# Kernel optimization log

Hardware: AMD Instinct MI355X
Metric: run time of the kernel (lower is better)

The kernel has to match this reference:

```python
import jax, jax.numpy as jnp
import numpy as np

NUM_HEADS = 16
INPUT_DIM = 1024
ATTENTION_DIM = 1024
DEPTH = ATTENTION_DIM // NUM_HEADS
NEG = -(2.0 ** 32) + 1.0  # large negative used by the original masking


def setup_inputs() -> dict:
    key = jax.random.key(0)
    kq, kk, k1, k2, k3 = jax.random.split(key, 5)
    B, L = 4, 1024
    s = 1.0 / np.sqrt(INPUT_DIM)
    return {
        "query": jax.random.normal(kq, (B, L, INPUT_DIM), dtype=jnp.float32),
        "key": jax.random.normal(kk, (B, L, INPUT_DIM), dtype=jnp.float32),
        "Wq": jax.random.normal(k1, (INPUT_DIM, ATTENTION_DIM), dtype=jnp.float32) * s,
        "Wk": jax.random.normal(k2, (INPUT_DIM, ATTENTION_DIM), dtype=jnp.float32) * s,
        "Wv": jax.random.normal(k3, (INPUT_DIM, ATTENTION_DIM), dtype=jnp.float32) * s,
    }


def reference(query, key, Wq, Wk, Wv):
    B, Lq, _ = query.shape
    Lk = key.shape[1]
    q = query @ Wq  # [B, Lq, A]
    k = key @ Wk    # [B, Lk, A]
    v = key @ Wv
    # Faithful to torch: raw row-major reshape [B, L, A] -> [B*H, L, depth]
    q_ = q.reshape(-1, Lq, DEPTH)
    k_ = k.reshape(-1, Lk, DEPTH)
    v_ = v.reshape(-1, Lk, DEPTH)
    scores = jnp.einsum('bid,bjd->bij', q_, k_) / (DEPTH ** 0.5)  # [BH, Lq, Lk]
    # key padding mask, tiled head-major like torch.tile(key_mask, [H, 1])
    key_mask = jnp.sign(jnp.abs(key.sum(-1)))           # [B, Lk]
    key_mask = jnp.tile(key_mask, (NUM_HEADS, 1))        # [HB, Lk]
    scores = jnp.where(key_mask[:, None, :] == 0, NEG, scores)
    # causal mask
    tril = jnp.tril(jnp.ones((Lq, Lk), dtype=scores.dtype))
    scores = jnp.where(tril[None] == 0, NEG, scores)
    attn = jax.nn.softmax(scores, axis=-1)
    # query mask: original tiles to [HB, Lk, Lq] and multiplies elementwise,
    # i.e. masks the LAST axis with the query mask (requires Lq == Lk)
    query_mask = jnp.sign(jnp.abs(query.sum(-1)))        # [B, Lq]
    query_mask = jnp.tile(query_mask, (NUM_HEADS, 1))    # [HB, Lq]
    attn = attn * query_mask[:, None, :]
    # dropout is identity in eval mode
    out = attn @ v_                                      # [BH, Lq, depth]
    out = jnp.concatenate(jnp.split(out, NUM_HEADS, axis=0), axis=-1)  # [B, Lq, A]
    out = out + query
    norm = jnp.sqrt(jnp.sum(out * out, axis=-1, keepdims=True))
    out = out / jnp.maximum(norm, 1e-12)
    return out
```

## Files before the change

kernel.cpp:

```cpp
#include <hip/hip_runtime.h>
#include <cstdint>
#include <cstddef>


#define US unsigned short

typedef __attribute__((ext_vector_type(4))) float f32x4;
typedef __attribute__((ext_vector_type(8))) short bf16x8;
typedef __attribute__((ext_vector_type(8))) US ushort8_t;
typedef __attribute__((ext_vector_type(4))) US ushort4_t;

__device__ __forceinline__ US f2bf(float f) {
  union { float f; uint32_t u; } c; c.f = f;
  uint32_t u = c.u;
  return (US)((u + 0x7FFFu + ((u >> 16) & 1u)) >> 16);
}

__device__ __forceinline__ uint32_t cvtpk(float lo, float hi) {
  uint32_t r;
  asm("v_cvt_pk_bf16_f32 %0, %1, %2" : "=v"(r) : "v"(lo), "v"(hi));
  return r;
}

__device__ __forceinline__ void gld16(const void* g, void* l) {
  __builtin_amdgcn_global_load_lds(
      (const __attribute__((address_space(1))) uint32_t*)g,
      (__attribute__((address_space(3))) uint32_t*)l, 16, 0, 0);
}

__global__ __launch_bounds__(256) void prep(const float* __restrict__ q,
                                            const float* __restrict__ k,
                                            US* __restrict__ qb,
                                            US* __restrict__ kb,
                                            const float* __restrict__ Wq,
                                            const float* __restrict__ Wk,
                                            const float* __restrict__ Wv,
                                            US* __restrict__ Tq,
                                            US* __restrict__ Tk,
                                            US* __restrict__ Tv) {
  const int bid = blockIdx.x;
  if (bid < 8192) {
    uint32_t i = bid * 256u + threadIdx.x;
    const bool isq = i < 1048576u;
    const float4* src = (const float4*)(isq ? q : k);
    US* dst = isq ? qb : kb;
    uint32_t j = isq ? i : i - 1048576u;
    float4 v = src[j];
    ushort4_t o = { f2bf(v.x), f2bf(v.y), f2bf(v.z), f2bf(v.w) };
    *(ushort4_t*)(dst + (size_t)j * 4) = o;
    return;
  }
  const int rem = bid - 8192;
  const int z = rem >> 8;
  const int r8 = rem & 255;
  const float* W = (z == 0) ? Wq : (z == 1) ? Wk : Wv;
  US* T = (z == 0) ? Tq : (z == 1) ? Tk : Tv;
  __shared__ float tile[64][65];
  const int r0 = (r8 >> 4) * 64, c0 = (r8 & 15) * 64;
  const int tx = threadIdx.x & 63, ty = threadIdx.x >> 6;
  #pragma unroll
  for (int rr = ty; rr < 64; rr += 4)
    tile[rr][tx] = W[(size_t)(r0 + rr) * 1024 + c0 + tx];
  __syncthreads();
  #pragma unroll
  for (int rr = ty; rr < 64; rr += 4)
    T[(size_t)(c0 + rr) * 1024 + r0 + tx] = f2bf(tile[tx][rr]);
}

__global__ __launch_bounds__(256) void gemm_qkv(
    const US* __restrict__ qin, const US* __restrict__ kin,
    const US* __restrict__ WqT, const US* __restrict__ WkT,
    const US* __restrict__ WvT,
    US* __restrict__ qo, US* __restrict__ ko, US* __restrict__ vo) {
  const int z = blockIdx.z;
  const US* A = (z == 0) ? qin : kin;
  const US* B = (z == 0) ? WqT : (z == 1) ? WkT : WvT;
  US* C = (z == 0) ? qo : (z == 1) ? ko : vo;

  __shared__ __align__(16) US Abuf[128 * 64];
  __shared__ __align__(16) US Bbuf[128 * 64];

  const int t = threadIdx.x;
  const int w = t >> 6, l = t & 63;
  const int lr = l & 15, lu = l >> 4;
  const int brow = blockIdx.x * 128;
  const int bcol = blockIdx.y * 128;
  const int wm = (w >> 1) * 64, wn = (w & 1) * 64;

  f32x4 acc[4][4] = {};

  for (int ks = 0; ks < 16; ++ks) {
    const int kb = ks * 64;
    #pragma unroll
    for (int rd = 0; rd < 4; ++rd) {
      const int s = rd * 256 + t;
      const int r = s >> 3;
      const int u = (l & 7) ^ (r & 7);
      const size_t lofs = (size_t)(rd * 256 + w * 64) * 16;
      gld16(A + (size_t)(brow + r) * 1024 + kb + u * 8, (char*)Abuf + lofs);
      gld16(B + (size_t)(bcol + r) * 1024 + kb + u * 8, (char*)Bbuf + lofs);
    }
    __syncthreads();

    #pragma unroll
    for (int kk = 0; kk < 2; ++kk) {
      bf16x8 af[4], bfr[4];
      #pragma unroll
      for (int mf = 0; mf < 4; ++mf) {
        const int ra = wm + mf * 16 + lr;
        af[mf] = *(const bf16x8*)((const char*)Abuf + ra * 128 +
                                  (((kk * 4 + lu) ^ (ra & 7)) * 16));
        const int rb = wn + mf * 16 + lr;
        bfr[mf] = *(const bf16x8*)((const char*)Bbuf + rb * 128 +
                                   (((kk * 4 + lu) ^ (rb & 7)) * 16));
      }
      __builtin_amdgcn_s_setprio(1);
      #pragma unroll
      for (int mf = 0; mf < 4; ++mf)
        #pragma unroll
        for (int nf = 0; nf < 4; ++nf)
          acc[mf][nf] = __builtin_amdgcn_mfma_f32_16x16x32_bf16(af[mf], bfr[nf],
                                                                acc[mf][nf], 0, 0, 0);
      __builtin_amdgcn_s_setprio(0);
    }
    __syncthreads();
  }

  #pragma unroll
  for (int mf = 0; mf < 4; ++mf)
    #pragma unroll
    for (int nf = 0; nf < 4; ++nf)
      #pragma unroll
      for (int i = 0; i < 4; ++i) {
        const int row = brow + wm + mf * 16 + lu * 4 + i;
        const int col = bcol + wn + nf * 16 + lr;
        C[(size_t)row * 1024 + col] = f2bf(acc[mf][nf][i]);
      }
}

__global__ __launch_bounds__(256) void vtrans(const US* __restrict__ v,
                                              US* __restrict__ vT) {
  const int g = blockIdx.x;
  const int kt = blockIdx.y;
  __shared__ __align__(16) US tile[64][72];
  const US* src = v + (size_t)g * 65536;
  US* dst = vT + (size_t)g * 65536;
  const int t = threadIdx.x;
  #pragma unroll
  for (int q = 0; q < 2; ++q) {
    const int s = q * 256 + t;
    const int key = s >> 3, dc = (s & 7) * 8;
    *(ushort8_t*)&tile[key][dc] =
        *(const ushort8_t*)(src + (size_t)(kt * 64 + key) * 64 + dc);
  }
  __syncthreads();
  #pragma unroll
  for (int i = 0; i < 16; ++i) {
    const int idx = i * 256 + t;
    const int d = idx >> 6, kl = idx & 63;
    dst[(size_t)d * 1024 + kt * 64 + kl] = tile[kl][d];
  }
}

__global__ __launch_bounds__(512, 4) void attn(const US* __restrict__ qbf,
                                               const US* __restrict__ kbf,
                                               const US* __restrict__ vT,
                                               float* __restrict__ ab) {
  const int x = blockIdx.x;
  const int g = x & 63;
  const int idx = x >> 6;
  const int s = (idx < 4) ? (7 - idx) : (idx - 4);
  const int w = threadIdx.x >> 6, l = threadIdx.x & 63;
  const int lr = l & 15, lu = l >> 4;
  const int i0 = s * 128 + w * 16;

  const US* Qg = qbf + (size_t)g * 65536;
  const US* Kg = kbf + (size_t)g * 65536;
  const US* Vg = vT + (size_t)g * 65536;

  __shared__ __align__(16) US Kt[2][64][64];
  __shared__ __align__(16) US Vt[2][64][64];
  __shared__ __align__(16) US Plds[8][16][72];

  bf16x8 qf[2];
  #pragma unroll
  for (int kc = 0; kc < 2; ++kc)
    qf[kc] = *(const bf16x8*)(Qg + (size_t)(i0 + lr) * 64 + kc * 32 + lu * 8);

  f32x4 o[4] = {};
  float lsp = 0.f;
  const float SC = 0.18033688011112042f;
  const float CB = 5.770780163555852f;

  const int ns_blk = 2 * s + 2;
  const int my_ns  = (i0 + 79) >> 6;

  const int srow = w * 8 + (l >> 3);
  const int sunit = (l & 7) ^ (srow & 7);
  auto stage = [&](int buf, int jb) {
    gld16(Kg + (size_t)(jb + srow) * 64 + sunit * 8, (char*)Kt[buf] + w * 1024);
    gld16(Vg + (size_t)srow * 1024 + jb + sunit * 8, (char*)Vt[buf] + w * 1024);
  };

  stage(0, 0);
  __syncthreads();

  for (int jt = 0; jt < ns_blk; ++jt) {
    const int buf = jt & 1;
    if (jt + 1 < ns_blk) stage(buf ^ 1, (jt + 1) * 64);

    if (jt < my_ns) {
      const int jb = jt * 64;
      f32x4 s4[4] = {};
      #pragma unroll
      for (int nt = 0; nt < 4; ++nt) {
        const int row = nt * 16 + lr;
        #pragma unroll
        for (int kc = 0; kc < 2; ++kc) {
          bf16x8 kf = *(const bf16x8*)((const char*)Kt[buf] + row * 128 +
                                       (((kc * 4 + lu) ^ (lr & 7)) * 16));
          s4[nt] = __builtin_amdgcn_mfma_f32_16x16x32_bf16(kf, qf[kc], s4[nt], 0, 0, 0);
        }
      }
      const int tdiag = i0 + lr - jb;
      #pragma unroll
      for (int nt = 0; nt < 4; ++nt) {
        float e[4];
        #pragma unroll
        for (int r = 0; r < 4; ++r) {
          float arg = s4[nt][r] * SC - CB;
          if (nt * 16 + lu * 4 + r > tdiag) arg = -__builtin_inff();
          e[r] = __builtin_amdgcn_exp2f(arg);
          lsp += e[r];
        }
        uint2 wv;
        wv.x = cvtpk(e[0], e[1]);
        wv.y = cvtpk(e[2], e[3]);
        *(uint2*)&Plds[w][lr][nt * 16 + lu * 4] = wv;
      }
      #pragma unroll
      for (int c = 0; c < 2; ++c) {
        bf16x8 pf = *(const bf16x8*)&Plds[w][lr][c * 32 + lu * 8];
        __builtin_amdgcn_s_setprio(1);
        #pragma unroll
        for (int dt = 0; dt < 4; ++dt) {
          const int vrow = dt * 16 + lr;
          bf16x8 vf = *(const bf16x8*)((const char*)Vt[buf] + vrow * 128 +
                                       (((c * 4 + lu) ^ (lr & 7)) * 16));
          o[dt] = __builtin_amdgcn_mfma_f32_16x16x32_bf16(vf, pf, o[dt], 0, 0, 0);
        }
        __builtin_amdgcn_s_setprio(0);
      }
    }
    __syncthreads();
  }

  float ls = lsp;
  ls += __shfl_xor(ls, 16);
  ls += __shfl_xor(ls, 32);
  const float inv = 1.0f / ls;
  const int i = i0 + lr;
  const size_t base = (size_t)(g & 3) * 1048576 + (size_t)i * 1024 + (g >> 2) * 64;
  #pragma unroll
  for (int dt = 0; dt < 4; ++dt) {
    f32x4 ov = o[dt] * inv;
    *(f32x4*)(ab + base + dt * 16 + lu * 4) = ov;
  }
}

__global__ __launch_bounds__(256) void epi(const float* __restrict__ ab,
                                           const float* __restrict__ query,
                                           float* __restrict__ out) {
  const int row = blockIdx.x;
  const int t = threadIdx.x;
  const float4 x = ((const float4*)(ab + (size_t)row * 1024))[t];
  const float4 y = ((const float4*)(query + (size_t)row * 1024))[t];
  float4 v;
  v.x = x.x + y.x; v.y = x.y + y.y; v.z = x.z + y.z; v.w = x.w + y.w;
  float ss = v.x * v.x + v.y * v.y + v.z * v.z + v.w * v.w;
  #pragma unroll
  for (int d = 1; d < 64; d <<= 1) ss += __shfl_xor(ss, d, 64);
  __shared__ float red[4];
  if ((t & 63) == 0) red[t >> 6] = ss;
  __syncthreads();
  const float tot = red[0] + red[1] + red[2] + red[3];
  const float inv = 1.0f / fmaxf(sqrtf(tot), 1e-12f);
  float4 o2;
  o2.x = v.x * inv; o2.y = v.y * inv; o2.z = v.z * inv; o2.w = v.w * inv;
  ((float4*)(out + (size_t)row * 1024))[t] = o2;
}

extern "C" void kernel_launch(void* const* d_in, const int* in_sizes, int n_in,
                              void* d_out, int out_size, void* d_ws, size_t ws_size,
                              hipStream_t stream) {
  const float* query = (const float*)d_in[0];
  const float* key   = (const float*)d_in[1];
  const float* Wq    = (const float*)d_in[2];
  const float* Wk    = (const float*)d_in[3];
  const float* Wv    = (const float*)d_in[4];
  float* out = (float*)d_out;

  char* ws = (char*)d_ws;
  const size_t MB = 1u << 20;
  US* query_bf = (US*)(ws + 0);
  US* key_bf   = (US*)(ws + 8 * MB);
  US* WqT = (US*)(ws + 16 * MB);
  US* WkT = (US*)(ws + 18 * MB);
  US* WvT = (US*)(ws + 20 * MB);
  US* q_bf = (US*)(ws + 22 * MB);
  US* k_bf = (US*)(ws + 30 * MB);
  US* v_bf = (US*)(ws + 38 * MB);
  US* vTb  = (US*)(ws + 46 * MB);
  float* ab = (float*)(ws + 0);

  prep<<<8960, 256, 0, stream>>>(query, key, query_bf, key_bf,
                                 Wq, Wk, Wv, WqT, WkT, WvT);
  gemm_qkv<<<dim3(32, 8, 3), 256, 0, stream>>>(query_bf, key_bf, WqT, WkT, WvT,
                                               q_bf, k_bf, v_bf);
  vtrans<<<dim3(64, 16), 256, 0, stream>>>(v_bf, vTb);
  attn<<<512, 512, 0, stream>>>(q_bf, k_bf, vTb, ab);
  epi<<<4096, 256, 0, stream>>>(ab, query, out);
}
```

Before: 81.87 us.

## Double-buffer QKV GEMM LDS tiles and skip causal masking on full attention tiles

Result: slower. 91.68 us (+12.0%).

```diff
diff --git a/kernel.cpp b/kernel.cpp
--- a/kernel.cpp
+++ b/kernel.cpp
@@ -77,8 +77,8 @@
   const US* B = (z == 0) ? WqT : (z == 1) ? WkT : WvT;
   US* C = (z == 0) ? qo : (z == 1) ? ko : vo;
 
-  __shared__ __align__(16) US Abuf[128 * 64];
-  __shared__ __align__(16) US Bbuf[128 * 64];
+  __shared__ __align__(16) US Abuf[2][128 * 64];
+  __shared__ __align__(16) US Bbuf[2][128 * 64];
 
   const int t = threadIdx.x;
   const int w = t >> 6, l = t & 63;
@@ -89,18 +89,24 @@
 
   f32x4 acc[4][4] = {};
 
-  for (int ks = 0; ks < 16; ++ks) {
-    const int kb = ks * 64;
+  auto stage = [&](int nb, int kb) {
     #pragma unroll
     for (int rd = 0; rd < 4; ++rd) {
       const int s = rd * 256 + t;
       const int r = s >> 3;
       const int u = (l & 7) ^ (r & 7);
       const size_t lofs = (size_t)(rd * 256 + w * 64) * 16;
-      gld16(A + (size_t)(brow + r) * 1024 + kb + u * 8, (char*)Abuf + lofs);
-      gld16(B + (size_t)(bcol + r) * 1024 + kb + u * 8, (char*)Bbuf + lofs);
-    }
-    __syncthreads();
+      gld16(A + (size_t)(brow + r) * 1024 + kb + u * 8, (char*)Abuf[nb] + lofs);
+      gld16(B + (size_t)(bcol + r) * 1024 + kb + u * 8, (char*)Bbuf[nb] + lofs);
+    }
+  };
+
+  stage(0, 0);
+  __syncthreads();
+
+  for (int ks = 0; ks < 16; ++ks) {
+    const int buf = ks & 1;
+    if (ks + 1 < 16) stage(buf ^ 1, (ks + 1) * 64);
 
     #pragma unroll
     for (int kk = 0; kk < 2; ++kk) {
@@ -108,10 +114,10 @@
       #pragma unroll
       for (int mf = 0; mf < 4; ++mf) {
         const int ra = wm + mf * 16 + lr;
-        af[mf] = *(const bf16x8*)((const char*)Abuf + ra * 128 +
+        af[mf] = *(const bf16x8*)((const char*)Abuf[buf] + ra * 128 +
                                   (((kk * 4 + lu) ^ (ra & 7)) * 16));
         const int rb = wn + mf * 16 + lr;
-        bfr[mf] = *(const bf16x8*)((const char*)Bbuf + rb * 128 +
+        bfr[mf] = *(const bf16x8*)((const char*)Bbuf[buf] + rb * 128 +
                                    (((kk * 4 + lu) ^ (rb & 7)) * 16));
       }
       __builtin_amdgcn_s_setprio(1);
@@ -193,7 +199,7 @@
   const float CB = 5.770780163555852f;
 
   const int ns_blk = 2 * s + 2;
-  const int my_ns  = (i0 + 79) >> 6;
+  const int nfull  = i0 >> 6;
 
   const int srow = w * 8 + (l >> 3);
   const int sunit = (l & 7) ^ (srow & 7);
@@ -202,56 +208,59 @@
     gld16(Vg + (size_t)srow * 1024 + jb + sunit * 8, (char*)Vt[buf] + w * 1024);
   };
 
+  auto body = [&](int buf, int jb, bool domask) {
+    f32x4 s4[4] = {};
+    #pragma unroll
+    for (int nt = 0; nt < 4; ++nt) {
+      const int row = nt * 16 + lr;
+      #pragma unroll
+      for (int kc = 0; kc < 2; ++kc) {
+        bf16x8 kf = *(const bf16x8*)((const char*)Kt[buf] + row * 128 +
+                                     (((kc * 4 + lu) ^ (lr & 7)) * 16));
+        __builtin_amdgcn_s_setprio(1);
+        s4[nt] = __builtin_amdgcn_mfma_f32_16x16x32_bf16(kf, qf[kc], s4[nt], 0, 0, 0);
+        __builtin_amdgcn_s_setprio(0);
+      }
+    }
+    const int tdiag = i0 + lr - jb;
+    #pragma unroll
+    for (int nt = 0; nt < 4; ++nt) {
+      float e[4];
+      #pragma unroll
+      for (int r = 0; r < 4; ++r) {
+        float arg = s4[nt][r] * SC - CB;
+        if (domask && (nt * 16 + lu * 4 + r > tdiag)) arg = -__builtin_inff();
+        e[r] = __builtin_amdgcn_exp2f(arg);
+        lsp += e[r];
+      }
+      uint2 wv;
+      wv.x = cvtpk(e[0], e[1]);
+      wv.y = cvtpk(e[2], e[3]);
+      *(uint2*)&Plds[w][lr][nt * 16 + lu * 4] = wv;
+    }
+    #pragma unroll
+    for (int c = 0; c < 2; ++c) {
+      bf16x8 pf = *(const bf16x8*)&Plds[w][lr][c * 32 + lu * 8];
+      __builtin_amdgcn_s_setprio(1);
+      #pragma unroll
+      for (int dt = 0; dt < 4; ++dt) {
+        const int vrow = dt * 16 + lr;
+        bf16x8 vf = *(const bf16x8*)((const char*)Vt[buf] + vrow * 128 +
+                                     (((c * 4 + lu) ^ (lr & 7)) * 16));
+        o[dt] = __builtin_amdgcn_mfma_f32_16x16x32_bf16(vf, pf, o[dt], 0, 0, 0);
+      }
+      __builtin_amdgcn_s_setprio(0);
+    }
+  };
+
   stage(0, 0);
   __syncthreads();
 
   for (int jt = 0; jt < ns_blk; ++jt) {
     const int buf = jt & 1;
     if (jt + 1 < ns_blk) stage(buf ^ 1, (jt + 1) * 64);
-
-    if (jt < my_ns) {
-      const int jb = jt * 64;
-      f32x4 s4[4] = {};
-      #pragma unroll
-      for (int nt = 0; nt < 4; ++nt) {
-        const int row = nt * 16 + lr;
-        #pragma unroll
-        for (int kc = 0; kc < 2; ++kc) {
-          bf16x8 kf = *(const bf16x8*)((const char*)Kt[buf] + row * 128 +
-                                       (((kc * 4 + lu) ^ (lr & 7)) * 16));
-          s4[nt] = __builtin_amdgcn_mfma_f32_16x16x32_bf16(kf, qf[kc], s4[nt], 0, 0, 0);
-        }
-      }
-      const int tdiag = i0 + lr - jb;
-      #pragma unroll
-      for (int nt = 0; nt < 4; ++nt) {
-        float e[4];
-        #pragma unroll
-        for (int r = 0; r < 4; ++r) {
-          float arg = s4[nt][r] * SC - CB;
-          if (nt * 16 + lu * 4 + r > tdiag) arg = -__builtin_inff();
-          e[r] = __builtin_amdgcn_exp2f(arg);
-          lsp += e[r];
-        }
-        uint2 wv;
-        wv.x = cvtpk(e[0], e[1]);
-        wv.y = cvtpk(e[2], e[3]);
-        *(uint2*)&Plds[w][lr][nt * 16 + lu * 4] = wv;
-      }
-      #pragma unroll
-      for (int c = 0; c < 2; ++c) {
-        bf16x8 pf = *(const bf16x8*)&Plds[w][lr][c * 32 + lu * 8];
-        __builtin_amdgcn_s_setprio(1);
-        #pragma unroll
-        for (int dt = 0; dt < 4; ++dt) {
-          const int vrow = dt * 16 + lr;
-          bf16x8 vf = *(const bf16x8*)((const char*)Vt[buf] + vrow * 128 +
-                                       (((c * 4 + lu) ^ (lr & 7)) * 16));
-          o[dt] = __builtin_amdgcn_mfma_f32_16x16x32_bf16(vf, pf, o[dt], 0, 0, 0);
-        }
-        __builtin_amdgcn_s_setprio(0);
-      }
-    }
+    if (jt < nfull)        body(buf, jt * 64, false);
+    else if (jt == nfull)  body(buf, jt * 64, true);
     __syncthreads();
   }
 
```

## Fuse K and V projections sharing the key tile; specialize unmasked attention tiles

Applied to the files above, without the earlier changes.

Result: slower. 99.46 us (+21.5%).

```diff
diff --git a/kernel.cpp b/kernel.cpp
--- a/kernel.cpp
+++ b/kernel.cpp
@@ -73,12 +73,13 @@
     const US* __restrict__ WvT,
     US* __restrict__ qo, US* __restrict__ ko, US* __restrict__ vo) {
   const int z = blockIdx.z;
-  const US* A = (z == 0) ? qin : kin;
-  const US* B = (z == 0) ? WqT : (z == 1) ? WkT : WvT;
-  US* C = (z == 0) ? qo : (z == 1) ? ko : vo;
+  const US* A  = (z == 0) ? qin : kin;
+  const US* B0 = (z == 0) ? WqT : WkT;
+  US* C0 = (z == 0) ? qo : ko;
 
   __shared__ __align__(16) US Abuf[128 * 64];
-  __shared__ __align__(16) US Bbuf[128 * 64];
+  __shared__ __align__(16) US B0buf[128 * 64];
+  __shared__ __align__(16) US B1buf[128 * 64];
 
   const int t = threadIdx.x;
   const int w = t >> 6, l = t & 63;
@@ -87,7 +88,8 @@
   const int bcol = blockIdx.y * 128;
   const int wm = (w >> 1) * 64, wn = (w & 1) * 64;
 
-  f32x4 acc[4][4] = {};
+  f32x4 acc0[4][4] = {};
+  f32x4 acc1[4][4] = {};
 
   for (int ks = 0; ks < 16; ++ks) {
     const int kb = ks * 64;
@@ -98,20 +100,22 @@
       const int u = (l & 7) ^ (r & 7);
       const size_t lofs = (size_t)(rd * 256 + w * 64) * 16;
       gld16(A + (size_t)(brow + r) * 1024 + kb + u * 8, (char*)Abuf + lofs);
-      gld16(B + (size_t)(bcol + r) * 1024 + kb + u * 8, (char*)Bbuf + lofs);
+      gld16(B0 + (size_t)(bcol + r) * 1024 + kb + u * 8, (char*)B0buf + lofs);
+      if (z)
+        gld16(WvT + (size_t)(bcol + r) * 1024 + kb + u * 8, (char*)B1buf + lofs);
     }
     __syncthreads();
 
     #pragma unroll
     for (int kk = 0; kk < 2; ++kk) {
-      bf16x8 af[4], bfr[4];
+      bf16x8 af[4], b0f[4];
       #pragma unroll
       for (int mf = 0; mf < 4; ++mf) {
         const int ra = wm + mf * 16 + lr;
         af[mf] = *(const bf16x8*)((const char*)Abuf + ra * 128 +
                                   (((kk * 4 + lu) ^ (ra & 7)) * 16));
         const int rb = wn + mf * 16 + lr;
-        bfr[mf] = *(const bf16x8*)((const char*)Bbuf + rb * 128 +
+        b0f[mf] = *(const bf16x8*)((const char*)B0buf + rb * 128 +
                                    (((kk * 4 + lu) ^ (rb & 7)) * 16));
       }
       __builtin_amdgcn_s_setprio(1);
@@ -119,9 +123,26 @@
       for (int mf = 0; mf < 4; ++mf)
         #pragma unroll
         for (int nf = 0; nf < 4; ++nf)
-          acc[mf][nf] = __builtin_amdgcn_mfma_f32_16x16x32_bf16(af[mf], bfr[nf],
-                                                                acc[mf][nf], 0, 0, 0);
+          acc0[mf][nf] = __builtin_amdgcn_mfma_f32_16x16x32_bf16(af[mf], b0f[nf],
+                                                                 acc0[mf][nf], 0, 0, 0);
       __builtin_amdgcn_s_setprio(0);
+      if (z) {
+        bf16x8 b1f[4];
+        #pragma unroll
+        for (int nf = 0; nf < 4; ++nf) {
+          const int rb = wn + nf * 16 + lr;
+          b1f[nf] = *(const bf16x8*)((const char*)B1buf + rb * 128 +
+                                     (((kk * 4 + lu) ^ (rb & 7)) * 16));
+        }
+        __builtin_amdgcn_s_setprio(1);
+        #pragma unroll
+        for (int mf = 0; mf < 4; ++mf)
+          #pragma unroll
+          for (int nf = 0; nf < 4; ++nf)
+            acc1[mf][nf] = __builtin_amdgcn_mfma_f32_16x16x32_bf16(af[mf], b1f[nf],
+                                                                   acc1[mf][nf], 0, 0, 0);
+        __builtin_amdgcn_s_setprio(0);
+      }
     }
     __syncthreads();
   }
@@ -134,7 +155,8 @@
       for (int i = 0; i < 4; ++i) {
         const int row = brow + wm + mf * 16 + lu * 4 + i;
         const int col = bcol + wn + nf * 16 + lr;
-        C[(size_t)row * 1024 + col] = f2bf(acc[mf][nf][i]);
+        C0[(size_t)row * 1024 + col] = f2bf(acc0[mf][nf][i]);
+        if (z) vo[(size_t)row * 1024 + col] = f2bf(acc1[mf][nf][i]);
       }
 }
 
@@ -193,7 +215,7 @@
   const float CB = 5.770780163555852f;
 
   const int ns_blk = 2 * s + 2;
-  const int my_ns  = (i0 + 79) >> 6;
+  const int nfull  = i0 >> 6;
 
   const int srow = w * 8 + (l >> 3);
   const int sunit = (l & 7) ^ (srow & 7);
@@ -202,56 +224,59 @@
     gld16(Vg + (size_t)srow * 1024 + jb + sunit * 8, (char*)Vt[buf] + w * 1024);
   };
 
+  auto body = [&](int buf, int jb, bool domask) {
+    f32x4 s4[4] = {};
+    #pragma unroll
+    for (int nt = 0; nt < 4; ++nt) {
+      const int row = nt * 16 + lr;
+      #pragma unroll
+      for (int kc = 0; kc < 2; ++kc) {
+        bf16x8 kf = *(const bf16x8*)((const char*)Kt[buf] + row * 128 +
+                                     (((kc * 4 + lu) ^ (lr & 7)) * 16));
+        __builtin_amdgcn_s_setprio(1);
+        s4[nt] = __builtin_amdgcn_mfma_f32_16x16x32_bf16(kf, qf[kc], s4[nt], 0, 0, 0);
+        __builtin_amdgcn_s_setprio(0);
+      }
+    }
+    const int tdiag = i0 + lr - jb;
+    #pragma unroll
+    for (int nt = 0; nt < 4; ++nt) {
+      float e[4];
+      #pragma unroll
+      for (int r = 0; r < 4; ++r) {
+        float arg = s4[nt][r] * SC - CB;
+        if (domask && (nt * 16 + lu * 4 + r > tdiag)) arg = -__builtin_inff();
+        e[r] = __builtin_amdgcn_exp2f(arg);
+        lsp += e[r];
+      }
+      uint2 wv;
+      wv.x = cvtpk(e[0], e[1]);
+      wv.y = cvtpk(e[2], e[3]);
+      *(uint2*)&Plds[w][lr][nt * 16 + lu * 4] = wv;
+    }
+    #pragma unroll
+    for (int c = 0; c < 2; ++c) {
+      bf16x8 pf = *(const bf16x8*)&Plds[w][lr][c * 32 + lu * 8];
+      __builtin_amdgcn_s_setprio(1);
+      #pragma unroll
+      for (int dt = 0; dt < 4; ++dt) {
+        const int vrow = dt * 16 + lr;
+        bf16x8 vf = *(const bf16x8*)((const char*)Vt[buf] + vrow * 128 +
+                                     (((c * 4 + lu) ^ (lr & 7)) * 16));
+        o[dt] = __builtin_amdgcn_mfma_f32_16x16x32_bf16(vf, pf, o[dt], 0, 0, 0);
+      }
+      __builtin_amdgcn_s_setprio(0);
+    }
+  };
+
   stage(0, 0);
   __syncthreads();
 
   for (int jt = 0; jt < ns_blk; ++jt) {
     const int buf = jt & 1;
     if (jt + 1 < ns_blk) stage(buf ^ 1, (jt + 1) * 64);
-
-    if (jt < my_ns) {
-      const int jb = jt * 64;
-      f32x4 s4[4] = {};
-      #pragma unroll
-      for (int nt = 0; nt < 4; ++nt) {
-        const int row = nt * 16 + lr;
-        #pragma unroll
-        for (int kc = 0; kc < 2; ++kc) {
-          bf16x8 kf = *(const bf16x8*)((const char*)Kt[buf] + row * 128 +
-                                       (((kc * 4 + lu) ^ (lr & 7)) * 16));
-          s4[nt] = __builtin_amdgcn_mfma_f32_16x16x32_bf16(kf, qf[kc], s4[nt], 0, 0, 0);
-        }
-      }
-      const int tdiag = i0 + lr - jb;
-      #pragma unroll
-      for (int nt = 0; nt < 4; ++nt) {
-        float e[4];
-        #pragma unroll
-        for (int r = 0; r < 4; ++r) {
-          float arg = s4[nt][r] * SC - CB;
-          if (nt * 16 + lu * 4 + r > tdiag) arg = -__builtin_inff();
-          e[r] = __builtin_amdgcn_exp2f(arg);
-          lsp += e[r];
-        }
-        uint2 wv;
-        wv.x = cvtpk(e[0], e[1]);
-        wv.y = cvtpk(e[2], e[3]);
-        *(uint2*)&Plds[w][lr][nt * 16 + lu * 4] = wv;
-      }
-      #pragma unroll
-      for (int c = 0; c < 2; ++c) {
-        bf16x8 pf = *(const bf16x8*)&Plds[w][lr][c * 32 + lu * 8];
-        __builtin_amdgcn_s_setprio(1);
-        #pragma unroll
-        for (int dt = 0; dt < 4; ++dt) {
-          const int vrow = dt * 16 + lr;
-          bf16x8 vf = *(const bf16x8*)((const char*)Vt[buf] + vrow * 128 +
-                                       (((c * 4 + lu) ^ (lr & 7)) * 16));
-          o[dt] = __builtin_amdgcn_mfma_f32_16x16x32_bf16(vf, pf, o[dt], 0, 0, 0);
-        }
-        __builtin_amdgcn_s_setprio(0);
-      }
-    }
+    if (jt < nfull)        body(buf, jt * 64, false);
+    else if (jt == nfull)  body(buf, jt * 64, true);
     __syncthreads();
   }
 
@@ -315,7 +340,7 @@
 
   prep<<<8960, 256, 0, stream>>>(query, key, query_bf, key_bf,
                                  Wq, Wk, Wv, WqT, WkT, WvT);
-  gemm_qkv<<<dim3(32, 8, 3), 256, 0, stream>>>(query_bf, key_bf, WqT, WkT, WvT,
+  gemm_qkv<<<dim3(32, 8, 2), 256, 0, stream>>>(query_bf, key_bf, WqT, WkT, WvT,
                                                q_bf, k_bf, v_bf);
   vtrans<<<dim3(64, 16), 256, 0, stream>>>(v_bf, vTb);
   attn<<<512, 512, 0, stream>>>(q_bf, k_bf, vTb, ab);
```
